# Performance work log

Hardware: AMD Instinct MI355X
Metric: run time of the kernel (lower is better)

## Reference

```python
import jax, jax.numpy as jnp
import numpy as np

EPS = 1e-5
NHEADS = 4
NLAYERS = 6

def layernorm(x, g, b):
    m = jnp.mean(x, axis=-1, keepdims=True)
    v = jnp.var(x, axis=-1, keepdims=True)
    return (x - m) * jax.lax.rsqrt(v + EPS) * g + b

def leaky_relu(x):
    return jnp.where(x >= 0, x, 0.1 * x)  # LeakyReLU(negative_slope=0.1)

def biased_mha(x, bias, mask, Wq, bq, Wk, bk, Wv, bv, Wo, bo):
    # dgl.nn.BiasedMHA: scores = (q/sqrt(dh)) k^T + bias (per-head), mask==True -> -inf
    B, N, D = x.shape
    dh = D // NHEADS
    q = (x @ Wq + bq).reshape(B, N, NHEADS, dh) * (dh ** -0.5)
    k = (x @ Wk + bk).reshape(B, N, NHEADS, dh)
    v = (x @ Wv + bv).reshape(B, N, NHEADS, dh)
    scores = jnp.einsum('bqhd,bkhd->bqkh', q, k) + bias  # [B,N,N,H]
    scores = jnp.where(mask[..., None], -jnp.inf, scores)
    w = jax.nn.softmax(scores, axis=2)  # softmax over keys
    out = jnp.einsum('bqkh,bkhd->bqhd', w, v).reshape(B, N, D)
    return out @ Wo + bo

def graphormer_forward(node_feat_new, attn_bias, deg_in_emb, deg_out_emb,
                       mlp_n_W1, mlp_n_b1, mlp_n_W2, mlp_n_b2,
                       Wq, bq, Wk, bk, Wv, bv, Wo, bo,
                       ln1_g, ln1_b, W1, b1, W2, b2, ln2_g, ln2_b,
                       mlp_out_W1, mlp_out_b1, mlp_out_W2, mlp_out_b2,
                       in_degree, out_degree, attn_mask, po_idx):
    # DegreeEncoder (directed): clamp to max_degree=8, sum of two embedding tables
    deg = deg_in_emb[jnp.clip(in_degree, 0, 8)] + deg_out_emb[jnp.clip(out_degree, 0, 8)]
    # mlp_n: Linear -> LeakyReLU(0.1) -> Linear
    h = leaky_relu(node_feat_new @ mlp_n_W1 + mlp_n_b1) @ mlp_n_W2 + mlp_n_b2
    x = h + deg
    mask = attn_mask != 0
    for i in range(NLAYERS):  # 6 GraphormerLayers, norm_first=False (post-norm)
        res = x
        a = biased_mha(x, attn_bias, mask, Wq[i], bq[i], Wk[i], bk[i], Wv[i], bv[i], Wo[i], bo[i])
        x = layernorm(res + a, ln1_g[i], ln1_b[i])
        res = x
        f = jax.nn.relu(x @ W1[i] + b1[i]) @ W2[i] + b2[i]  # FFN with ReLU
        x = layernorm(res + f, ln2_g[i], ln2_b[i])
    B = x.shape[0]
    sel = x[jnp.arange(B)[:, None], po_idx].reshape(-1, x.shape[-1])  # gather PO nodes
    return leaky_relu(sel @ mlp_out_W1 + mlp_out_b1) @ mlp_out_W2 + mlp_out_b2

def setup_inputs():
    B, N, F_IN, D, HID, P, L = 8, 1024, 64, 512, 1024, 128, 6
    key = jax.random.key(0)
    ks = jax.random.split(key, 32)
    def w(k, shape, fan_in):
        return jax.random.normal(k, shape, jnp.float32) / np.float32(np.sqrt(fan_in))
    return dict(
        node_feat_new=jax.random.normal(ks[0], (B, N, F_IN), jnp.float32),
        in_degree=jax.random.randint(ks[1], (B, N), 0, 9),
        out_degree=jax.random.randint(ks[2], (B, N), 0, 9),
        dist=jax.random.randint(ks[3], (B, N, N), 0, 6).astype(jnp.int32),
        attn_mask=jax.random.randint(ks[4], (B, N, N), 0, 2).astype(jnp.int32),
        po_idx=jax.random.randint(ks[5], (B, P), 0, N),
        attn_bias=jax.random.uniform(ks[6], (B, N, N, NHEADS), jnp.float32),
        deg_in_emb=w(ks[7], (9, D), D),
        deg_out_emb=w(ks[8], (9, D), D),
        mlp_n_W1=w(ks[9], (F_IN, D // 2), F_IN), mlp_n_b1=jnp.zeros((D // 2,), jnp.float32),
        mlp_n_W2=w(ks[10], (D // 2, D), D // 2), mlp_n_b2=jnp.zeros((D,), jnp.float32),
        Wq=w(ks[11], (L, D, D), D), bq=jnp.zeros((L, D), jnp.float32),
        Wk=w(ks[12], (L, D, D), D), bk=jnp.zeros((L, D), jnp.float32),
        Wv=w(ks[13], (L, D, D), D), bv=jnp.zeros((L, D), jnp.float32),
        Wo=w(ks[14], (L, D, D), D), bo=jnp.zeros((L, D), jnp.float32),
        ln1_g=jnp.ones((L, D), jnp.float32), ln1_b=jnp.zeros((L, D), jnp.float32),
        W1=w(ks[15], (L, D, HID), D), b1=jnp.zeros((L, HID), jnp.float32),
        W2=w(ks[16], (L, HID, D), HID), b2=jnp.zeros((L, D), jnp.float32),
        ln2_g=jnp.ones((L, D), jnp.float32), ln2_b=jnp.zeros((L, D), jnp.float32),
        mlp_out_W1=w(ks[17], (D, D // 2), D), mlp_out_b1=jnp.zeros((D // 2,), jnp.float32),
        mlp_out_W2=w(ks[18], (D // 2, 1), D // 2), mlp_out_b2=jnp.zeros((1,), jnp.float32),
    )

def reference(node_feat_new, in_degree, out_degree, dist, attn_mask, po_idx, attn_bias,
              deg_in_emb, deg_out_emb, mlp_n_W1, mlp_n_b1, mlp_n_W2, mlp_n_b2,
              Wq, bq, Wk, bk, Wv, bv, Wo, bo, ln1_g, ln1_b, W1, b1, W2, b2, ln2_g, ln2_b,
              mlp_out_W1, mlp_out_b1, mlp_out_W2, mlp_out_b2):
    del dist  # original computes spatial encoding from dist but overwrites attn_bias with rand (dead code)
    return graphormer_forward(node_feat_new, attn_bias, deg_in_emb, deg_out_emb,
                              mlp_n_W1, mlp_n_b1, mlp_n_W2, mlp_n_b2,
                              Wq, bq, Wk, bk, Wv, bv, Wo, bo,
                              ln1_g, ln1_b, W1, b1, W2, b2, ln2_g, ln2_b,
                              mlp_out_W1, mlp_out_b1, mlp_out_W2, mlp_out_b2,
                              in_degree, out_degree, attn_mask, po_idx)
```

## Files before the change

### kernel.cpp

```cpp
#include <hip/hip_runtime.h>

typedef unsigned short u16;
typedef unsigned int u32;
typedef short bf16x8 __attribute__((ext_vector_type(8)));
typedef float f32x4 __attribute__((ext_vector_type(4)));

__device__ __forceinline__ float us2f(u16 u) {
  union { unsigned int i; float f; } x; x.i = ((unsigned int)u) << 16; return x.f;
}
__device__ __forceinline__ u16 f2bf(float f) {
  union { float f; unsigned int i; } x; x.f = f;
  unsigned int i = x.i;
  return (u16)((i + 0x7FFFu + ((i >> 16) & 1u)) >> 16);
}
__device__ __forceinline__ int probe_f32(const void* p) {
  return ((const u16*)p)[0] == 0;
}
__device__ __forceinline__ float ldf(const void* p, size_t i, int f32) {
  return f32 ? ((const float*)p)[i] : us2f(((const u16*)p)[i]);
}
__device__ __forceinline__ float4 ldf4(const void* p, size_t i, int f32) {
  if (f32) return *(const float4*)((const float*)p + i);
  const ushort4 t = *(const ushort4*)((const u16*)p + i);
  return make_float4(us2f(t.x), us2f(t.y), us2f(t.z), us2f(t.w));
}

template <int BN, int BK>
__global__ __launch_bounds__(256) void gemm_mfma_t(
    const void* __restrict__ probe, const void* __restrict__ A, int a_mode,
    int lda, const void* __restrict__ W, size_t wOff,
    const void* __restrict__ bias, size_t bOff, const u16* __restrict__ res,
    void* __restrict__ C, int c_bf16, int M, int N, int K, int act) {
  const int in_f32 = probe_f32(probe);
  const int a_f32 = (a_mode == 2) ? in_f32 : 0;
  constexpr int NT = BN / 16;
  constexpr int KH = BK / 32;
  constexpr int KPAIRS = BK / 2;
  constexpr int NW = BN * BK / 512;
  constexpr int LDK = BK + 8;
  __shared__ u16 As[2][128][LDK];
  __shared__ u16 Bt[2][BN][LDK];
  const int tid = threadIdx.x;
  const int n0 = blockIdx.x * BN, m0 = blockIdx.y * 128;
  const int wv = tid >> 6, lane = tid & 63;
  const int lk = lane & 15, quad = lane >> 4;
  const int wm = wv * 32;

  f32x4 acc[2][NT];
#pragma unroll
  for (int i = 0; i < 2; i++)
#pragma unroll
    for (int j = 0; j < NT; j++) acc[i][j] = (f32x4){0.f, 0.f, 0.f, 0.f};

  const int sar = tid >> 1, sac = (tid & 1) * (BK / 2);
  const int kp = tid % KPAIRS, nseg = tid / KPAIRS;

  u16 abuf[BK / 2];
  u32 wbuf[NW];
  auto loadA = [&](int k0) {
    if (a_f32) {
      const float* ap = (const float*)A + (size_t)(m0 + sar) * lda + k0 + sac;
#pragma unroll
      for (int q = 0; q < BK / 8; q++) {
        const float4 f = *(const float4*)(ap + q * 4);
        abuf[q * 4 + 0] = f2bf(f.x); abuf[q * 4 + 1] = f2bf(f.y);
        abuf[q * 4 + 2] = f2bf(f.z); abuf[q * 4 + 3] = f2bf(f.w);
      }
    } else {
      const u16* ap = (const u16*)A + (size_t)(m0 + sar) * lda + k0 + sac;
#pragma unroll
      for (int q = 0; q < BK / 16; q++)
        *(bf16x8*)&abuf[q * 8] = *(const bf16x8*)(ap + q * 8);
    }
  };
  auto loadW = [&](int k0) {
    const size_t wb = wOff + (size_t)(k0 + 2 * kp) * N + n0 + nseg * NW;
    if (in_f32) {
      const float* wp = (const float*)W + wb;
#pragma unroll
      for (int i = 0; i < NW; i++)
        wbuf[i] = ((u32)f2bf(wp[N + i]) << 16) | (u32)f2bf(wp[i]);
    } else {
      const u16* wp = (const u16*)W + wb;
#pragma unroll
      for (int i = 0; i < NW; i++)
        wbuf[i] = ((u32)wp[N + i] << 16) | (u32)wp[i];
    }
  };
  auto store = [&](int bi) {
#pragma unroll
    for (int q = 0; q < BK / 16; q++)
      *(bf16x8*)&As[bi][sar][sac + q * 8] = *(bf16x8*)&abuf[q * 8];
#pragma unroll
    for (int i = 0; i < NW; i++) *(u32*)&Bt[bi][nseg * NW + i][2 * kp] = wbuf[i];
  };

  const int nk = K / BK;
  loadA(0); loadW(0); store(0);
  __syncthreads();
  for (int kt = 0; kt < nk; kt++) {
    const int cur = kt & 1;
    if (kt + 1 < nk) { loadA((kt + 1) * BK); loadW((kt + 1) * BK); }
    bf16x8 af[2][KH], bfv[NT][KH];
#pragma unroll
    for (int i = 0; i < 2; i++)
#pragma unroll
      for (int h = 0; h < KH; h++)
        af[i][h] = *(const bf16x8*)&As[cur][wm + i * 16 + lk][h * 32 + quad * 8];
#pragma unroll
    for (int j = 0; j < NT; j++)
#pragma unroll
      for (int h = 0; h < KH; h++)
        bfv[j][h] = *(const bf16x8*)&Bt[cur][j * 16 + lk][h * 32 + quad * 8];
#pragma unroll
    for (int i = 0; i < 2; i++)
#pragma unroll
      for (int j = 0; j < NT; j++)
#pragma unroll
        for (int h = 0; h < KH; h++)
          acc[i][j] = __builtin_amdgcn_mfma_f32_16x16x32_bf16(
              af[i][h], bfv[j][h], acc[i][j], 0, 0, 0);
    if (kt + 1 < nk) store(cur ^ 1);
    __syncthreads();
  }

#pragma unroll
  for (int j = 0; j < NT; j++) {
    const int col = n0 + j * 16 + lk;
    const float bb = bias ? ldf(bias, bOff + col, in_f32) : 0.f;
#pragma unroll
    for (int i = 0; i < 2; i++) {
#pragma unroll
      for (int r = 0; r < 4; r++) {
        const int row = m0 + wm + i * 16 + quad * 4 + r;
        float t = acc[i][j][r] + bb;
        if (act == 1) t = t > 0.f ? t : 0.f;
        else if (act == 2) t = t >= 0.f ? t : 0.1f * t;
        if (res) t += us2f(res[(size_t)row * N + col]);
        if (c_bf16) ((u16*)C)[(size_t)row * N + col] = f2bf(t);
        else ((float*)C)[(size_t)row * N + col] = t;
      }
    }
  }
}

__global__ __launch_bounds__(256) void gemm_qkv(
    const void* __restrict__ probe, const u16* __restrict__ A,
    const void* __restrict__ Wq, const void* __restrict__ Wk,
    const void* __restrict__ Wv, size_t wOff, const void* __restrict__ bq,
    const void* __restrict__ bk, const void* __restrict__ bv, size_t bOff,
    u16* __restrict__ C) {
  const int in_f32 = probe_f32(probe);
  __shared__ u16 As[2][128][40];
  __shared__ u16 Bt[2][128][40];
  const int tid = threadIdx.x;
  const int n0 = blockIdx.x * 128, m0 = blockIdx.y * 128;
  const int src = n0 >> 9, nn0 = n0 & 511;
  const void* W = src == 0 ? Wq : (src == 1 ? Wk : Wv);
  const void* bias = src == 0 ? bq : (src == 1 ? bk : bv);
  const int wv = tid >> 6, lane = tid & 63;
  const int lk = lane & 15, quad = lane >> 4;
  const int wm = wv * 32;

  f32x4 acc[2][8];
#pragma unroll
  for (int i = 0; i < 2; i++)
#pragma unroll
    for (int j = 0; j < 8; j++) acc[i][j] = (f32x4){0.f, 0.f, 0.f, 0.f};

  const int sar = tid >> 1, sac = (tid & 1) * 16;
  const int kp = tid & 15, nseg = tid >> 4;

  u16 abuf[16];
  u32 wbuf[8];
  auto loadA = [&](int k0) {
    const u16* ap = A + (size_t)(m0 + sar) * 512 + k0 + sac;
    *(bf16x8*)&abuf[0] = *(const bf16x8*)ap;
    *(bf16x8*)&abuf[8] = *(const bf16x8*)(ap + 8);
  };
  auto loadW = [&](int k0) {
    const size_t wb = wOff + (size_t)(k0 + 2 * kp) * 512 + nn0 + nseg * 8;
    if (in_f32) {
      const float* wp = (const float*)W + wb;
#pragma unroll
      for (int i = 0; i < 8; i++)
        wbuf[i] = ((u32)f2bf(wp[512 + i]) << 16) | (u32)f2bf(wp[i]);
    } else {
      const u16* wp = (const u16*)W + wb;
#pragma unroll
      for (int i = 0; i < 8; i++)
        wbuf[i] = ((u32)wp[512 + i] << 16) | (u32)wp[i];
    }
  };
  auto store = [&](int bi) {
    *(bf16x8*)&As[bi][sar][sac] = *(bf16x8*)&abuf[0];
    *(bf16x8*)&As[bi][sar][sac + 8] = *(bf16x8*)&abuf[8];
#pragma unroll
    for (int i = 0; i < 8; i++) *(u32*)&Bt[bi][nseg * 8 + i][2 * kp] = wbuf[i];
  };

  loadA(0); loadW(0); store(0);
  __syncthreads();
  for (int kt = 0; kt < 16; kt++) {
    const int cur = kt & 1;
    if (kt < 15) { loadA((kt + 1) * 32); loadW((kt + 1) * 32); }
    bf16x8 af[2], bfv[8];
#pragma unroll
    for (int i = 0; i < 2; i++)
      af[i] = *(const bf16x8*)&As[cur][wm + i * 16 + lk][quad * 8];
#pragma unroll
    for (int j = 0; j < 8; j++)
      bfv[j] = *(const bf16x8*)&Bt[cur][j * 16 + lk][quad * 8];
#pragma unroll
    for (int i = 0; i < 2; i++)
#pragma unroll
      for (int j = 0; j < 8; j++)
        acc[i][j] = __builtin_amdgcn_mfma_f32_16x16x32_bf16(af[i], bfv[j],
                                                            acc[i][j], 0, 0, 0);
    if (kt < 15) store(cur ^ 1);
    __syncthreads();
  }

#pragma unroll
  for (int j = 0; j < 8; j++) {
    const int coll = nn0 + j * 16 + lk;
    const float bb = ldf(bias, bOff + coll, in_f32);
#pragma unroll
    for (int i = 0; i < 2; i++) {
#pragma unroll
      for (int r = 0; r < 4; r++) {
        const int row = m0 + wm + i * 16 + quad * 4 + r;
        C[(size_t)row * 1536 + n0 + j * 16 + lk] = f2bf(acc[i][j][r] + bb);
      }
    }
  }
}

__global__ __launch_bounds__(256) void deg_kernel(const void* __restrict__ probe,
    u16* __restrict__ x, const int* __restrict__ ind, const int* __restrict__ outd,
    const void* __restrict__ ein, const void* __restrict__ eout) {
  const int f32 = probe_f32(probe);
  const int r = blockIdx.x, tid = threadIdx.x;
  int a = ind[r]; a = a < 0 ? 0 : (a > 8 ? 8 : a);
  int b = outd[r]; b = b < 0 ? 0 : (b > 8 ? 8 : b);
  const size_t base = (size_t)r * 512;
  for (int c = tid; c < 512; c += 256) {
    const float v = us2f(x[base + c]) + ldf(ein, (size_t)a * 512 + c, f32) +
                    ldf(eout, (size_t)b * 512 + c, f32);
    x[base + c] = f2bf(v);
  }
}

__global__ __launch_bounds__(256) void bias_pack(const void* __restrict__ probe,
    const void* __restrict__ bias, const int* __restrict__ mask,
    u16* __restrict__ biasm) {
  const int f32 = probe_f32(probe);
  __shared__ u16 pl[4][1032];
  const int bq = blockIdx.x, t = threadIdx.x;
  const size_t rk = (size_t)bq * 1024;
  const u16 NB = f2bf(-3.0e38f);
#pragma unroll
  for (int j = 0; j < 4; j++) {
    const int k = t + j * 256;
    const int mv = mask[rk + k];
    float h0, h1, h2, h3;
    if (f32) {
      const float4 f = *(const float4*)((const float*)bias + (rk + k) * 4);
      h0 = f.x; h1 = f.y; h2 = f.z; h3 = f.w;
    } else {
      const ushort4 u = *(const ushort4*)((const u16*)bias + (rk + k) * 4);
      h0 = us2f(u.x); h1 = us2f(u.y); h2 = us2f(u.z); h3 = us2f(u.w);
    }
    pl[0][k] = mv ? NB : f2bf(h0);
    pl[1][k] = mv ? NB : f2bf(h1);
    pl[2][k] = mv ? NB : f2bf(h2);
    pl[3][k] = mv ? NB : f2bf(h3);
  }
  __syncthreads();
  const int b = bq >> 10, q = bq & 1023;
  const int p = t & 3, seg = t >> 2;
  u16* dst = biasm + (((size_t)(b * 4 + p)) << 20) + (size_t)q * 1024 + seg * 16;
  *(bf16x8*)dst = *(const bf16x8*)&pl[p][seg * 16];
  *(bf16x8*)(dst + 8) = *(const bf16x8*)&pl[p][seg * 16 + 8];
}

__global__ __launch_bounds__(256) void attn_mfma(const void* __restrict__ probe,
    const u16* __restrict__ QKV, const void* __restrict__ bias,
    const int* __restrict__ mask, u16* __restrict__ O,
    const u16* __restrict__ biasm) {
  const int f32 = probe_f32(probe);
  __shared__ u16 Kls[2][32][136];
  __shared__ u16 Vt[2][128][40];
  __shared__ u16 Pl[4][16][40];
  const int b = blockIdx.z, h = blockIdx.y, q0 = blockIdx.x * 64;
  const int tid = threadIdx.x;
  const int wv = tid >> 6, lane = tid & 63;
  const int lk = lane & 15, quad = lane >> 4;
  const float scale = 0.08838834764831845f;
  const float NEG = -3.0e38f;

  const size_t qg = (size_t)(b * 1024 + q0 + wv * 16);
  const int lq = q0 + wv * 16;
  const u16* bm = biasm ? biasm + (((size_t)(b * 4 + h)) << 20) : (const u16*)0;

  bf16x8 qf[4];
#pragma unroll
  for (int c = 0; c < 4; c++)
    qf[c] = *(const bf16x8*)(QKV + (qg + lk) * 1536 + h * 128 + c * 32 + quad * 8);

  f32x4 o[8];
#pragma unroll
  for (int c = 0; c < 8; c++) o[c] = (f32x4){0.f, 0.f, 0.f, 0.f};
  float m_st[4], l_st[4];
#pragma unroll
  for (int r = 0; r < 4; r++) { m_st[r] = NEG; l_st[r] = 0.f; }

  const int kp = tid & 15, dseg = tid >> 4;

  bf16x8 ka, kb2, va, vb2;
  auto loadKV = [&](int k0) {
    const size_t r0 = (size_t)(b * 1024 + k0 + 2 * kp) * 1536 + h * 128 + dseg * 8;
    ka  = *(const bf16x8*)(QKV + r0 + 512);
    kb2 = *(const bf16x8*)(QKV + r0 + 512 + 1536);
    va  = *(const bf16x8*)(QKV + r0 + 1024);
    vb2 = *(const bf16x8*)(QKV + r0 + 1024 + 1536);
  };
  auto storeKV = [&](int bi) {
    *(bf16x8*)&Kls[bi][2 * kp][dseg * 8] = ka;
    *(bf16x8*)&Kls[bi][2 * kp + 1][dseg * 8] = kb2;
#pragma unroll
    for (int i = 0; i < 8; i++) {
      const unsigned int pk =
          ((unsigned int)(u16)vb2[i] << 16) | (unsigned int)(u16)va[i];
      *(unsigned int*)&Vt[bi][dseg * 8 + i][2 * kp] = pk;
    }
  };

  loadKV(0); storeKV(0);
  __syncthreads();

  for (int kt = 0; kt < 32; kt++) {
    const int cur = kt & 1;
    const int k0 = kt * 32;
    if (kt < 31) loadKV((kt + 1) * 32);

    float bv[2][4];
    if (bm) {
#pragma unroll
      for (int kh = 0; kh < 2; kh++)
#pragma unroll
        for (int r = 0; r < 4; r++)
          bv[kh][r] =
              us2f(bm[(size_t)(lq + quad * 4 + r) * 1024 + (k0 + kh * 16 + lk)]);
    }

    f32x4 sa[2];
#pragma unroll
    for (int kh = 0; kh < 2; kh++) {
      sa[kh] = (f32x4){0.f, 0.f, 0.f, 0.f};
#pragma unroll
      for (int c = 0; c < 4; c++) {
        const bf16x8 kf = *(const bf16x8*)&Kls[cur][kh * 16 + lk][c * 32 + quad * 8];
        sa[kh] = __builtin_amdgcn_mfma_f32_16x16x32_bf16(qf[c], kf, sa[kh], 0, 0, 0);
      }
    }
    float sv[2][4];
    if (bm) {
#pragma unroll
      for (int kh = 0; kh < 2; kh++)
#pragma unroll
        for (int r = 0; r < 4; r++)
          sv[kh][r] = sa[kh][r] * scale + bv[kh][r];
    } else {
#pragma unroll
      for (int kh = 0; kh < 2; kh++)
#pragma unroll
        for (int r = 0; r < 4; r++) {
          const size_t bidx = (qg + quad * 4 + r) * 1024 + (size_t)(k0 + kh * 16 + lk);
          const float s = sa[kh][r] * scale + ldf(bias, bidx * 4 + h, f32);
          sv[kh][r] = mask[bidx] ? NEG : s;
        }
    }
#pragma unroll
    for (int r = 0; r < 4; r++) {
      float lm = fmaxf(sv[0][r], sv[1][r]);
      lm = fmaxf(lm, __shfl_xor(lm, 1));
      lm = fmaxf(lm, __shfl_xor(lm, 2));
      lm = fmaxf(lm, __shfl_xor(lm, 4));
      lm = fmaxf(lm, __shfl_xor(lm, 8));
      const float mn = fmaxf(m_st[r], lm);
      const float al = __expf(m_st[r] - mn);
      const float p0 = (sv[0][r] <= -1e37f) ? 0.f : __expf(sv[0][r] - mn);
      const float p1 = (sv[1][r] <= -1e37f) ? 0.f : __expf(sv[1][r] - mn);
      float ts = p0 + p1;
      ts += __shfl_xor(ts, 1);
      ts += __shfl_xor(ts, 2);
      ts += __shfl_xor(ts, 4);
      ts += __shfl_xor(ts, 8);
      m_st[r] = mn;
      l_st[r] = l_st[r] * al + ts;
      Pl[wv][quad * 4 + r][lk] = f2bf(p0);
      Pl[wv][quad * 4 + r][16 + lk] = f2bf(p1);
#pragma unroll
      for (int c = 0; c < 8; c++) o[c][r] *= al;
    }
    const bf16x8 pa = *(const bf16x8*)&Pl[wv][lk][quad * 8];
#pragma unroll
    for (int c = 0; c < 8; c++) {
      const bf16x8 vf = *(const bf16x8*)&Vt[cur][c * 16 + lk][quad * 8];
      o[c] = __builtin_amdgcn_mfma_f32_16x16x32_bf16(pa, vf, o[c], 0, 0, 0);
    }
    if (kt < 31) storeKV(cur ^ 1);
    __syncthreads();
  }
#pragma unroll
  for (int r = 0; r < 4; r++) {
    const float invl = 1.f / fmaxf(l_st[r], 1e-20f);
    u16* op = O + (qg + quad * 4 + r) * 1536 + h * 128;
#pragma unroll
    for (int c = 0; c < 8; c++) op[c * 16 + lk] = f2bf(o[c][r] * invl);
  }
}

__global__ __launch_bounds__(256) void ln_kernel(const void* __restrict__ probe,
    const u16* __restrict__ in, const void* __restrict__ g,
    const void* __restrict__ bta, size_t gOff, u16* __restrict__ out) {
  const int f32 = probe_f32(probe);
  const int lane = threadIdx.x & 63, w = threadIdx.x >> 6;
  const size_t r = (size_t)blockIdx.x * 4 + w;
  const size_t base = r * 512 + lane * 8;
  const bf16x8 v = *(const bf16x8*)(in + base);
  float xv[8];
  float s = 0.f, sq = 0.f;
#pragma unroll
  for (int i = 0; i < 8; i++) {
    xv[i] = us2f((u16)v[i]);
    s += xv[i]; sq += xv[i] * xv[i];
  }
#pragma unroll
  for (int off = 32; off > 0; off >>= 1) {
    s += __shfl_xor(s, off);
    sq += __shfl_xor(sq, off);
  }
  const float m = s * (1.f / 512.f);
  const float var = fmaxf(sq * (1.f / 512.f) - m * m, 0.f);
  const float rs = rsqrtf(var + 1e-5f);
  const float4 g0 = ldf4(g, gOff + lane * 8, f32);
  const float4 g1 = ldf4(g, gOff + lane * 8 + 4, f32);
  const float4 b0 = ldf4(bta, gOff + lane * 8, f32);
  const float4 b1 = ldf4(bta, gOff + lane * 8 + 4, f32);
  const float gg[8] = {g0.x, g0.y, g0.z, g0.w, g1.x, g1.y, g1.z, g1.w};
  const float bb[8] = {b0.x, b0.y, b0.z, b0.w, b1.x, b1.y, b1.z, b1.w};
  bf16x8 ov;
#pragma unroll
  for (int i = 0; i < 8; i++) ov[i] = (short)f2bf((xv[i] - m) * rs * gg[i] + bb[i]);
  *(bf16x8*)(out + base) = ov;
}

__global__ __launch_bounds__(256) void final_kernel(const void* __restrict__ probe,
    const u16* __restrict__ x, const int* __restrict__ po,
    const void* __restrict__ W1, const void* __restrict__ b1,
    const void* __restrict__ W2, const void* __restrict__ b2,
    void* __restrict__ out) {
  const int f32 = probe_f32(probe);
  __shared__ float rsr[512];
  __shared__ float red[256];
  const int r = blockIdx.x, tid = threadIdx.x;
  const int b = r >> 7, p = r & 127;
  int n = po[b * 128 + p]; n = n < 0 ? 0 : (n > 1023 ? 1023 : n);
  const u16* row = x + ((size_t)(b * 1024 + n)) * 512;
  rsr[tid] = us2f(row[tid]); rsr[tid + 256] = us2f(row[tid + 256]);
  __syncthreads();
  float t = ldf(b1, tid, f32);
  for (int k = 0; k < 512; k++) t += rsr[k] * ldf(W1, (size_t)k * 256 + tid, f32);
  t = t >= 0.f ? t : 0.1f * t;
  red[tid] = t * ldf(W2, tid, f32);
  __syncthreads();
  for (int off = 128; off > 0; off >>= 1) {
    if (tid < off) red[tid] += red[tid + off];
    __syncthreads();
  }
  if (tid == 0) {
    const float v = red[0] + ldf(b2, 0, f32);
    if (f32) ((float*)out)[r] = v; else ((u16*)out)[r] = f2bf(v);
  }
}

extern "C" void kernel_launch(void* const* d_in, const int* in_sizes, int n_in,
                              void* d_out, int out_size, void* d_ws, size_t ws_size,
                              hipStream_t stream) {
  (void)in_sizes; (void)out_size;
  const int D = 512, HID = 1024, L = 6;
  const int M = 8192;

  const int sh = (n_in >= 33) ? 0 : 1;
#define IN(k) d_in[(k) - (((k) >= 4) ? sh : 0)]
  const void* nf   = IN(0);
  const int* ind   = (const int*)IN(1);
  const int* outd  = (const int*)IN(2);
  const int* amask = (const int*)IN(4);
  const int* po    = (const int*)IN(5);
  const void* abias = IN(6);
  const void* ein  = IN(7);
  const void* eout = IN(8);
  const void* mnW1 = IN(9);  const void* mnb1 = IN(10);
  const void* mnW2 = IN(11); const void* mnb2 = IN(12);
  const void* Wq = IN(13); const void* bq = IN(14);
  const void* Wk = IN(15); const void* bk = IN(16);
  const void* Wv = IN(17); const void* bv = IN(18);
  const void* Wo = IN(19); const void* bo = IN(20);
  const void* ln1g = IN(21); const void* ln1b = IN(22);
  const void* W1 = IN(23); const void* b1 = IN(24);
  const void* W2 = IN(25); const void* b2 = IN(26);
  const void* ln2g = IN(27); const void* ln2b = IN(28);
  const void* oW1 = IN(29); const void* ob1 = IN(30);
  const void* oW2 = IN(31); const void* ob2 = IN(32);
#undef IN
  const void* probe = ln1g;

  char* wsb = (char*)d_ws;
  u16* x   = (u16*)wsb;
  u16* yb  = (u16*)(wsb + ((size_t)8 << 20));
  u16* qkv = (u16*)(wsb + ((size_t)16 << 20));
  u16* h1b = yb;
  u16* hidb = qkv;
  u16* biasm = (ws_size >= ((size_t)104 << 20))
                   ? (u16*)(wsb + ((size_t)40 << 20)) : (u16*)0;

  dim3 blk(256);
  if (biasm) bias_pack<<<8192, blk, 0, stream>>>(probe, abias, amask, biasm);
  gemm_mfma_t<64, 64><<<dim3(4, M / 128), blk, 0, stream>>>(probe, nf, 2, 64, mnW1, 0, mnb1, 0, nullptr, h1b, 1, M, 256, 64, 2);
  gemm_mfma_t<64, 64><<<dim3(8, M / 128), blk, 0, stream>>>(probe, h1b, 1, 256, mnW2, 0, mnb2, 0, nullptr, x, 1, M, D, 256, 0);
  deg_kernel<<<M, blk, 0, stream>>>(probe, x, ind, outd, ein, eout);

  for (int l = 0; l < L; l++) {
    const size_t wO = (size_t)l * D * D, bO = (size_t)l * D;
    const size_t w1O = (size_t)l * D * HID, b1O = (size_t)l * HID;
    gemm_qkv<<<dim3(12, M / 128), blk, 0, stream>>>(probe, x, Wq, Wk, Wv, wO, bq, bk, bv, bO, qkv);
    attn_mfma<<<dim3(16, 4, 8), blk, 0, stream>>>(probe, qkv, abias, amask, qkv, biasm);
    gemm_mfma_t<64, 64><<<dim3(D / 64, M / 128), blk, 0, stream>>>(probe, qkv, 1, 1536, Wo, wO, bo, bO, x, yb, 1, M, D, D, 0);
    ln_kernel<<<M / 4, blk, 0, stream>>>(probe, yb, ln1g, ln1b, bO, x);
    gemm_mfma_t<128, 32><<<dim3(HID / 128, M / 128), blk, 0, stream>>>(probe, x, 1, 512, W1, w1O, b1, b1O, nullptr, hidb, 1, M, HID, D, 1);
    gemm_mfma_t<64, 64><<<dim3(D / 64, M / 128), blk, 0, stream>>>(probe, hidb, 1, 1024, W2, w1O, b2, bO, x, yb, 1, M, D, HID, 0);
    ln_kernel<<<M / 4, blk, 0, stream>>>(probe, yb, ln2g, ln2b, bO, x);
  }
  final_kernel<<<1024, blk, 0, stream>>>(probe, x, po, oW1, ob1, oW2, ob2, d_out);
}
```

Measured before the change: 1.770 ms.

## Pre-transpose weights to bf16 N-major and add lazy softmax rescale in attention

Adds per-layer weight conversion kernels that transpose and cast all weight matrices and biases to bf16 in an N-major layout in workspace. The GEMMs then load B tiles with contiguous 16-byte vector reads instead of strided scalar pair-packing, and the dedicated QKV kernel is replaced by the generic one. Attention also skips the running-max update and the output rescale when the new block max stays within 8 of the old max. The cost is one extra conversion kernel launch per layer plus extra workspace, and the lazy rescale lets exponentials grow up to e^8, which could affect accuracy.

```diff
diff --git a/kernel.cpp b/kernel.cpp
--- a/kernel.cpp
+++ b/kernel.cpp
@@ -25,19 +25,106 @@
   return make_float4(us2f(t.x), us2f(t.y), us2f(t.z), us2f(t.w));
 }
 
+__device__ __forceinline__ void tconv(u16 (*t)[72], const void* W, size_t off,
+    int K, int N, u16* dst, int k0, int n0, int f32, int tid) {
+  const int rr = tid >> 2, rc = (tid & 3) * 16;
+  const size_t src = off + (size_t)(k0 + rr) * N + n0 + rc;
+  u16 tmp[16];
+  if (f32) {
+    const float* p = (const float*)W + src;
+#pragma unroll
+    for (int q = 0; q < 4; q++) {
+      const float4 f = *(const float4*)(p + q * 4);
+      tmp[q * 4 + 0] = f2bf(f.x); tmp[q * 4 + 1] = f2bf(f.y);
+      tmp[q * 4 + 2] = f2bf(f.z); tmp[q * 4 + 3] = f2bf(f.w);
+    }
+  } else {
+    const u16* p = (const u16*)W + src;
+    *(bf16x8*)&tmp[0] = *(const bf16x8*)p;
+    *(bf16x8*)&tmp[8] = *(const bf16x8*)(p + 8);
+  }
+#pragma unroll
+  for (int j = 0; j < 16; j++) t[rr][rc + j] = tmp[j];
+  __syncthreads();
+  const int wr = tid >> 2, wc = (tid & 3) * 16;
+  u16 ot[16];
+#pragma unroll
+  for (int j = 0; j < 16; j++) ot[j] = t[wc + j][wr];
+  u16* d = dst + (size_t)(n0 + wr) * K + k0 + wc;
+  *(bf16x8*)d = *(bf16x8*)&ot[0];
+  *(bf16x8*)(d + 8) = *(bf16x8*)&ot[8];
+}
+
+__global__ __launch_bounds__(256) void wconv_layer(const void* __restrict__ probe,
+    const void* __restrict__ Wq, const void* __restrict__ Wk,
+    const void* __restrict__ Wv, const void* __restrict__ Wo,
+    const void* __restrict__ W1, const void* __restrict__ W2,
+    const void* __restrict__ bq, const void* __restrict__ bk,
+    const void* __restrict__ bv, const void* __restrict__ bo,
+    const void* __restrict__ b1, const void* __restrict__ b2,
+    size_t wO, size_t w1O, size_t bO, size_t b1O, u16* __restrict__ wt) {
+  const int f32 = probe_f32(probe);
+  __shared__ u16 t[64][72];
+  const int bid = blockIdx.x, tid = threadIdx.x;
+  if (bid < 192) {
+    const int src = bid / 64, tt = bid % 64;
+    const void* W = src == 0 ? Wq : (src == 1 ? Wk : Wv);
+    tconv(t, W, wO, 512, 512, wt + src * 262144, (tt & 7) * 64, (tt >> 3) * 64, f32, tid);
+  } else if (bid < 256) {
+    const int tt = bid - 192;
+    tconv(t, Wo, wO, 512, 512, wt + 786432, (tt & 7) * 64, (tt >> 3) * 64, f32, tid);
+  } else if (bid < 384) {
+    const int tt = bid - 256;
+    tconv(t, W1, w1O, 512, 1024, wt + 1048576, (tt & 7) * 64, (tt >> 3) * 64, f32, tid);
+  } else if (bid < 512) {
+    const int tt = bid - 384;
+    tconv(t, W2, w1O, 1024, 512, wt + 1572864, (tt & 15) * 64, (tt >> 4) * 64, f32, tid);
+  } else {
+    for (int i = tid; i < 4608; i += 256) {
+      float v;
+      if (i < 1536) {
+        const int s = i >> 9, c = i & 511;
+        v = ldf(s == 0 ? bq : (s == 1 ? bk : bv), bO + c, f32);
+      } else if (i < 2048) v = ldf(bo, bO + (i - 1536), f32);
+      else if (i < 3072) v = ldf(b1, b1O + (i - 2048), f32);
+      else v = ldf(b2, bO + (i - 3072), f32);
+      wt[2097152 + i] = f2bf(v);
+    }
+  }
+}
+
+__global__ __launch_bounds__(256) void wconv_node(const void* __restrict__ probe,
+    const void* __restrict__ mnW1, const void* __restrict__ mnW2,
+    const void* __restrict__ mnb1, const void* __restrict__ mnb2,
+    u16* __restrict__ wt) {
+  const int f32 = probe_f32(probe);
+  __shared__ u16 t[64][72];
+  const int bid = blockIdx.x, tid = threadIdx.x;
+  if (bid < 4) {
+    tconv(t, mnW1, 0, 64, 256, wt, 0, bid * 64, f32, tid);
+  } else if (bid < 36) {
+    const int tt = bid - 4;
+    tconv(t, mnW2, 0, 256, 512, wt + 16384, (tt & 3) * 64, (tt >> 2) * 64, f32, tid);
+  } else {
+    for (int i = tid; i < 768; i += 256) {
+      const float v = (i < 256) ? ldf(mnb1, i, f32) : ldf(mnb2, i - 256, f32);
+      wt[147456 + i] = f2bf(v);
+    }
+  }
+}
+
 template <int BN, int BK>
-__global__ __launch_bounds__(256) void gemm_mfma_t(
+__global__ __launch_bounds__(256) void gemm_bt(
     const void* __restrict__ probe, const void* __restrict__ A, int a_mode,
-    int lda, const void* __restrict__ W, size_t wOff,
-    const void* __restrict__ bias, size_t bOff, const u16* __restrict__ res,
-    void* __restrict__ C, int c_bf16, int M, int N, int K, int act) {
+    int lda, const u16* __restrict__ Wt, const u16* __restrict__ bias,
+    const u16* __restrict__ res, void* __restrict__ C, int c_bf16, int M,
+    int N, int K, int act) {
   const int in_f32 = probe_f32(probe);
   const int a_f32 = (a_mode == 2) ? in_f32 : 0;
   constexpr int NT = BN / 16;
   constexpr int KH = BK / 32;
-  constexpr int KPAIRS = BK / 2;
-  constexpr int NW = BN * BK / 512;
   constexpr int LDK = BK + 8;
+  constexpr int TPR = 256 / BN;
   __shared__ u16 As[2][128][LDK];
   __shared__ u16 Bt[2][BN][LDK];
   const int tid = threadIdx.x;
@@ -53,10 +140,9 @@
     for (int j = 0; j < NT; j++) acc[i][j] = (f32x4){0.f, 0.f, 0.f, 0.f};
 
   const int sar = tid >> 1, sac = (tid & 1) * (BK / 2);
-  const int kp = tid % KPAIRS, nseg = tid / KPAIRS;
-
-  u16 abuf[BK / 2];
-  u32 wbuf[NW];
+  const int br = tid / TPR, bc = (tid % TPR) * 16;
+
+  u16 abuf[BK / 2], bbuf[16];
   auto loadA = [&](int k0) {
     if (a_f32) {
       const float* ap = (const float*)A + (size_t)(m0 + sar) * lda + k0 + sac;
@@ -74,25 +160,16 @@
     }
   };
   auto loadW = [&](int k0) {
-    const size_t wb = wOff + (size_t)(k0 + 2 * kp) * N + n0 + nseg * NW;
-    if (in_f32) {
-      const float* wp = (const float*)W + wb;
-#pragma unroll
-      for (int i = 0; i < NW; i++)
-        wbuf[i] = ((u32)f2bf(wp[N + i]) << 16) | (u32)f2bf(wp[i]);
-    } else {
-      const u16* wp = (const u16*)W + wb;
-#pragma unroll
-      for (int i = 0; i < NW; i++)
-        wbuf[i] = ((u32)wp[N + i] << 16) | (u32)wp[i];
-    }
+    const u16* p = Wt + (size_t)(n0 + br) * K + k0 + bc;
+    *(bf16x8*)&bbuf[0] = *(const bf16x8*)p;
+    *(bf16x8*)&bbuf[8] = *(const bf16x8*)(p + 8);
   };
   auto store = [&](int bi) {
 #pragma unroll
     for (int q = 0; q < BK / 16; q++)
       *(bf16x8*)&As[bi][sar][sac + q * 8] = *(bf16x8*)&abuf[q * 8];
-#pragma unroll
-    for (int i = 0; i < NW; i++) *(u32*)&Bt[bi][nseg * NW + i][2 * kp] = wbuf[i];
+    *(bf16x8*)&Bt[bi][br][bc] = *(bf16x8*)&bbuf[0];
+    *(bf16x8*)&Bt[bi][br][bc + 8] = *(bf16x8*)&bbuf[8];
   };
 
   const int nk = K / BK;
@@ -127,7 +204,7 @@
 #pragma unroll
   for (int j = 0; j < NT; j++) {
     const int col = n0 + j * 16 + lk;
-    const float bb = bias ? ldf(bias, bOff + col, in_f32) : 0.f;
+    const float bb = bias ? us2f(bias[col]) : 0.f;
 #pragma unroll
     for (int i = 0; i < 2; i++) {
 #pragma unroll
@@ -139,98 +216,6 @@
         if (res) t += us2f(res[(size_t)row * N + col]);
         if (c_bf16) ((u16*)C)[(size_t)row * N + col] = f2bf(t);
         else ((float*)C)[(size_t)row * N + col] = t;
-      }
-    }
-  }
-}
-
-__global__ __launch_bounds__(256) void gemm_qkv(
-    const void* __restrict__ probe, const u16* __restrict__ A,
-    const void* __restrict__ Wq, const void* __restrict__ Wk,
-    const void* __restrict__ Wv, size_t wOff, const void* __restrict__ bq,
-    const void* __restrict__ bk, const void* __restrict__ bv, size_t bOff,
-    u16* __restrict__ C) {
-  const int in_f32 = probe_f32(probe);
-  __shared__ u16 As[2][128][40];
-  __shared__ u16 Bt[2][128][40];
-  const int tid = threadIdx.x;
-  const int n0 = blockIdx.x * 128, m0 = blockIdx.y * 128;
-  const int src = n0 >> 9, nn0 = n0 & 511;
-  const void* W = src == 0 ? Wq : (src == 1 ? Wk : Wv);
-  const void* bias = src == 0 ? bq : (src == 1 ? bk : bv);
-  const int wv = tid >> 6, lane = tid & 63;
-  const int lk = lane & 15, quad = lane >> 4;
-  const int wm = wv * 32;
-
-  f32x4 acc[2][8];
-#pragma unroll
-  for (int i = 0; i < 2; i++)
-#pragma unroll
-    for (int j = 0; j < 8; j++) acc[i][j] = (f32x4){0.f, 0.f, 0.f, 0.f};
-
-  const int sar = tid >> 1, sac = (tid & 1) * 16;
-  const int kp = tid & 15, nseg = tid >> 4;
-
-  u16 abuf[16];
-  u32 wbuf[8];
-  auto loadA = [&](int k0) {
-    const u16* ap = A + (size_t)(m0 + sar) * 512 + k0 + sac;
-    *(bf16x8*)&abuf[0] = *(const bf16x8*)ap;
-    *(bf16x8*)&abuf[8] = *(const bf16x8*)(ap + 8);
-  };
-  auto loadW = [&](int k0) {
-    const size_t wb = wOff + (size_t)(k0 + 2 * kp) * 512 + nn0 + nseg * 8;
-    if (in_f32) {
-      const float* wp = (const float*)W + wb;
-#pragma unroll
-      for (int i = 0; i < 8; i++)
-        wbuf[i] = ((u32)f2bf(wp[512 + i]) << 16) | (u32)f2bf(wp[i]);
-    } else {
-      const u16* wp = (const u16*)W + wb;
-#pragma unroll
-      for (int i = 0; i < 8; i++)
-        wbuf[i] = ((u32)wp[512 + i] << 16) | (u32)wp[i];
-    }
-  };
-  auto store = [&](int bi) {
-    *(bf16x8*)&As[bi][sar][sac] = *(bf16x8*)&abuf[0];
-    *(bf16x8*)&As[bi][sar][sac + 8] = *(bf16x8*)&abuf[8];
-#pragma unroll
-    for (int i = 0; i < 8; i++) *(u32*)&Bt[bi][nseg * 8 + i][2 * kp] = wbuf[i];
-  };
-
-  loadA(0); loadW(0); store(0);
-  __syncthreads();
-  for (int kt = 0; kt < 16; kt++) {
-    const int cur = kt & 1;
-    if (kt < 15) { loadA((kt + 1) * 32); loadW((kt + 1) * 32); }
-    bf16x8 af[2], bfv[8];
-#pragma unroll
-    for (int i = 0; i < 2; i++)
-      af[i] = *(const bf16x8*)&As[cur][wm + i * 16 + lk][quad * 8];
-#pragma unroll
-    for (int j = 0; j < 8; j++)
-      bfv[j] = *(const bf16x8*)&Bt[cur][j * 16 + lk][quad * 8];
-#pragma unroll
-    for (int i = 0; i < 2; i++)
-#pragma unroll
-      for (int j = 0; j < 8; j++)
-        acc[i][j] = __builtin_amdgcn_mfma_f32_16x16x32_bf16(af[i], bfv[j],
-                                                            acc[i][j], 0, 0, 0);
-    if (kt < 15) store(cur ^ 1);
-    __syncthreads();
-  }
-
-#pragma unroll
-  for (int j = 0; j < 8; j++) {
-    const int coll = nn0 + j * 16 + lk;
-    const float bb = ldf(bias, bOff + coll, in_f32);
-#pragma unroll
-    for (int i = 0; i < 2; i++) {
-#pragma unroll
-      for (int r = 0; r < 4; r++) {
-        const int row = m0 + wm + i * 16 + quad * 4 + r;
-        C[(size_t)row * 1536 + n0 + j * 16 + lk] = f2bf(acc[i][j][r] + bb);
       }
     }
   }
@@ -388,21 +373,34 @@
       lm = fmaxf(lm, __shfl_xor(lm, 2));
       lm = fmaxf(lm, __shfl_xor(lm, 4));
       lm = fmaxf(lm, __shfl_xor(lm, 8));
-      const float mn = fmaxf(m_st[r], lm);
-      const float al = __expf(m_st[r] - mn);
-      const float p0 = (sv[0][r] <= -1e37f) ? 0.f : __expf(sv[0][r] - mn);
-      const float p1 = (sv[1][r] <= -1e37f) ? 0.f : __expf(sv[1][r] - mn);
-      float ts = p0 + p1;
-      ts += __shfl_xor(ts, 1);
-      ts += __shfl_xor(ts, 2);
-      ts += __shfl_xor(ts, 4);
-      ts += __shfl_xor(ts, 8);
-      m_st[r] = mn;
-      l_st[r] = l_st[r] * al + ts;
-      Pl[wv][quad * 4 + r][lk] = f2bf(p0);
-      Pl[wv][quad * 4 + r][16 + lk] = f2bf(p1);
-#pragma unroll
-      for (int c = 0; c < 8; c++) o[c][r] *= al;
+      if (__all(lm - m_st[r] <= 8.f)) {
+        const float p0 = (sv[0][r] <= -1e37f) ? 0.f : __expf(sv[0][r] - m_st[r]);
+        const float p1 = (sv[1][r] <= -1e37f) ? 0.f : __expf(sv[1][r] - m_st[r]);
+        float ts = p0 + p1;
+        ts += __shfl_xor(ts, 1);
+        ts += __shfl_xor(ts, 2);
+        ts += __shfl_xor(ts, 4);
+        ts += __shfl_xor(ts, 8);
+        l_st[r] += ts;
+        Pl[wv][quad * 4 + r][lk] = f2bf(p0);
+        Pl[wv][quad * 4 + r][16 + lk] = f2bf(p1);
+      } else {
+        const float mn = fmaxf(m_st[r], lm);
+        const float al = __expf(m_st[r] - mn);
+        const float p0 = (sv[0][r] <= -1e37f) ? 0.f : __expf(sv[0][r] - mn);
+        const float p1 = (sv[1][r] <= -1e37f) ? 0.f : __expf(sv[1][r] - mn);
+        float ts = p0 + p1;
+        ts += __shfl_xor(ts, 1);
+        ts += __shfl_xor(ts, 2);
+        ts += __shfl_xor(ts, 4);
+        ts += __shfl_xor(ts, 8);
+        m_st[r] = mn;
+        l_st[r] = l_st[r] * al + ts;
+        Pl[wv][quad * 4 + r][lk] = f2bf(p0);
+        Pl[wv][quad * 4 + r][16 + lk] = f2bf(p1);
+#pragma unroll
+        for (int c = 0; c < 8; c++) o[c][r] *= al;
+      }
     }
     const bf16x8 pa = *(const bf16x8*)&Pl[wv][lk][quad * 8];
 #pragma unroll
@@ -522,26 +520,30 @@
   u16* x   = (u16*)wsb;
   u16* yb  = (u16*)(wsb + ((size_t)8 << 20));
   u16* qkv = (u16*)(wsb + ((size_t)16 << 20));
+  u16* wt  = (u16*)(wsb + ((size_t)40 << 20));
   u16* h1b = yb;
   u16* hidb = qkv;
-  u16* biasm = (ws_size >= ((size_t)104 << 20))
-                   ? (u16*)(wsb + ((size_t)40 << 20)) : (u16*)0;
+  u16* biasm = (ws_size >= ((size_t)109 << 20))
+                   ? (u16*)(wsb + ((size_t)45 << 20)) : (u16*)0;
 
   dim3 blk(256);
   if (biasm) bias_pack<<<8192, blk, 0, stream>>>(probe, abias, amask, biasm);
-  gemm_mfma_t<64, 64><<<dim3(4, M / 128), blk, 0, stream>>>(probe, nf, 2, 64, mnW1, 0, mnb1, 0, nullptr, h1b, 1, M, 256, 64, 2);
-  gemm_mfma_t<64, 64><<<dim3(8, M / 128), blk, 0, stream>>>(probe, h1b, 1, 256, mnW2, 0, mnb2, 0, nullptr, x, 1, M, D, 256, 0);
+  wconv_node<<<37, blk, 0, stream>>>(probe, mnW1, mnW2, mnb1, mnb2, wt);
+  gemm_bt<64, 64><<<dim3(4, M / 128), blk, 0, stream>>>(probe, nf, 2, 64, wt, wt + 147456, nullptr, h1b, 1, M, 256, 64, 2);
+  gemm_bt<64, 64><<<dim3(8, M / 128), blk, 0, stream>>>(probe, h1b, 1, 256, wt + 16384, wt + 147456 + 256, nullptr, x, 1, M, D, 256, 0);
   deg_kernel<<<M, blk, 0, stream>>>(probe, x, ind, outd, ein, eout);
 
   for (int l = 0; l < L; l++) {
     const size_t wO = (size_t)l * D * D, bO = (size_t)l * D;
     const size_t w1O = (size_t)l * D * HID, b1O = (size_t)l * HID;
-    gemm_qkv<<<dim3(12, M / 128), blk, 0, stream>>>(probe, x, Wq, Wk, Wv, wO, bq, bk, bv, bO, qkv);
+    wconv_layer<<<513, blk, 0, stream>>>(probe, Wq, Wk, Wv, Wo, W1, W2,
+                                         bq, bk, bv, bo, b1, b2, wO, w1O, bO, b1O, wt);
+    gemm_bt<128, 32><<<dim3(12, M / 128), blk, 0, stream>>>(probe, x, 1, 512, wt, wt + 2097152, nullptr, qkv, 1, M, 1536, 512, 0);
     attn_mfma<<<dim3(16, 4, 8), blk, 0, stream>>>(probe, qkv, abias, amask, qkv, biasm);
-    gemm_mfma_t<64, 64><<<dim3(D / 64, M / 128), blk, 0, stream>>>(probe, qkv, 1, 1536, Wo, wO, bo, bO, x, yb, 1, M, D, D, 0);
+    gemm_bt<64, 64><<<dim3(8, M / 128), blk, 0, stream>>>(probe, qkv, 1, 1536, wt + 786432, wt + 2097152 + 1536, x, yb, 1, M, D, D, 0);
     ln_kernel<<<M / 4, blk, 0, stream>>>(probe, yb, ln1g, ln1b, bO, x);
-    gemm_mfma_t<128, 32><<<dim3(HID / 128, M / 128), blk, 0, stream>>>(probe, x, 1, 512, W1, w1O, b1, b1O, nullptr, hidb, 1, M, HID, D, 1);
-    gemm_mfma_t<64, 64><<<dim3(D / 64, M / 128), blk, 0, stream>>>(probe, hidb, 1, 1024, W2, w1O, b2, bO, x, yb, 1, M, D, HID, 0);
+    gemm_bt<128, 32><<<dim3(8, M / 128), blk, 0, stream>>>(probe, x, 1, 512, wt + 1048576, wt + 2097152 + 2048, nullptr, hidb, 1, M, HID, 512, 1);
+    gemm_bt<64, 64><<<dim3(8, M / 128), blk, 0, stream>>>(probe, hidb, 1, 1024, wt + 1572864, wt + 2097152 + 3072, x, yb, 1, M, D, HID, 0);
     ln_kernel<<<M / 4, blk, 0, stream>>>(probe, yb, ln2g, ln2b, bO, x);
   }
   final_kernel<<<1024, blk, 0, stream>>>(probe, x, po, oW1, ob1, oW2, ob2, d_out);
```

Measured after the change: 2.235 ms. +26.3%, slower.
